# Performance work log

Measured on AMD Instinct MI355X. Metric: run time of the kernel, lower is better.

## Reference

```python
import jax, jax.numpy as jnp
import numpy as np

B, S, HID = 2, 1024, 2048
NH, NKV, D = 16, 8, 128
EPS = 1e-4 / 65535.0  # observer eps from ConcatObserver


def _ste(x, dq):
    # straight-through estimator used by torch fake-quant
    return x + jax.lax.stop_gradient(dq - x)


def _fq_range(x, mn, mx):
    # 16-bit per-tensor affine quantize-dequantize over a given range
    scale = jnp.maximum((mx - mn) / 65535.0, EPS)
    zp = jnp.round(-mn / scale)
    q = jnp.clip(jnp.round(x / scale) + zp, 0.0, 65535.0)
    return _ste(x, (q - zp) * scale)


def fq16(x):
    # ActivationQDQ(bits=16), per-tensor affine, zero included in range
    mn = jnp.minimum(jnp.min(x), 0.0)
    mx = jnp.maximum(jnp.max(x), 0.0)
    return _fq_range(x, mn, mx)


def fq8_sym(x):
    # ActivationQDQ(bits=8, per_tensor_symmetric)
    scale = jnp.maximum(jnp.max(jnp.abs(x)) / 127.0, 1e-12)
    q = jnp.clip(jnp.round(x / scale), -128.0, 127.0)
    return _ste(x, q * scale)


def lpbq_linear(x, W, block=32, qmax=7.0):
    # QLinearLPBQ: int4 weights with per-(out, block-of-32-inputs) scales, no bias
    O, I = W.shape
    Wb = W.reshape(O, I // block, block)
    s = jnp.maximum(jnp.max(jnp.abs(Wb), axis=-1, keepdims=True) / qmax, 1e-12)
    Wq = (jnp.clip(jnp.round(Wb / s), -qmax - 1.0, qmax) * s).reshape(O, I)
    return x @ _ste(W, Wq).T


def rmsnorm_fq(x, w, eps=1e-6):
    # QRMSNorm(head_dim, quant_bits=16)
    var = jnp.mean(x * x, axis=-1, keepdims=True)
    return fq16(x * jax.lax.rsqrt(var + eps) * w)


def rotate_half_fq(x):
    # rotate_half with neg-half QDQ and concat observer (range = union of observed tensors)
    d = x.shape[-1] // 2
    x1, x2 = x[..., :d], x[..., d:]
    neg = fq16(-x2)
    mn = jnp.minimum(jnp.minimum(jnp.min(x), jnp.min(neg)), 0.0)
    mx = jnp.maximum(jnp.maximum(jnp.max(x), jnp.max(neg)), 0.0)
    return _fq_range(jnp.concatenate([neg, x1], axis=-1), mn, mx)


def _attn_forward(hidden_states, cos, sin, attention_mask, Wq, Wk, Wv, Wo, q_norm_w, k_norm_w):
    scaling = D ** -0.5
    hs = fq16(hidden_states)                                            # q_proj_input_qdq
    q = fq16(lpbq_linear(hs, Wq)).reshape(B, S, NH, D)                  # q_norm_input_qdq
    q = jnp.transpose(rmsnorm_fq(q, q_norm_w), (0, 2, 1, 3))            # [B,NH,S,D]
    k = fq16(lpbq_linear(hs, Wk)).reshape(B, S, NKV, D)                 # k_norm_input_qdq
    k = jnp.transpose(rmsnorm_fq(k, k_norm_w), (0, 2, 1, 3))            # [B,NKV,S,D]
    v = jnp.transpose(lpbq_linear(hs, Wv).reshape(B, S, NKV, D), (0, 2, 1, 3))
    q = fq16(q)                                                         # q_norm_output_qdq
    k = fq16(k)                                                         # k_norm_output_qdq
    c = cos[:, None, :, :]
    s_ = sin[:, None, :, :]
    q = fq16(fq16(q * c) + fq16(rotate_half_fq(q) * s_))                # q RoPE with QDQs
    k = fq16(fq16(k * c) + fq16(rotate_half_fq(k) * s_))                # k RoPE with QDQs
    k = fq8_sym(k)                                                      # k_cast_to_int8_qdq
    v = fq8_sym(fq16(v))                                                # v int16 then int8 QDQ
    k = jnp.repeat(k, NH // NKV, axis=1)                                # repeat_kv
    v = jnp.repeat(v, NH // NKV, axis=1)
    sc = fq16(jnp.full((1,), scaling, dtype=hs.dtype))                  # scaling_qdq
    attn = fq16(fq16(jnp.einsum('bhsd,bhtd->bhst', q, k)) * sc)         # qk_matmul + mul_0
    amin = fq16(jnp.min(attn, axis=-1, keepdims=True))                  # reduce_min_output_qdq
    vv = fq16(amin + fq16(jnp.full((1,), -20.0, dtype=hs.dtype)))       # minus_0 (+ neg_20)
    attn = fq16(jnp.where(attention_mask == 0, attn, vv))               # where_attn_qdq
    attn = fq16(jax.nn.softmax(attn.astype(jnp.float32), axis=-1).astype(hs.dtype))
    out = fq16(jnp.einsum('bhst,bhtd->bhsd', attn, v))                  # attn_value_matmul
    out = jnp.transpose(out, (0, 2, 1, 3)).reshape(B, S, NH * D)
    return lpbq_linear(out, Wo), attn


def setup_inputs() -> dict:
    key = jax.random.key(0)
    ks = jax.random.split(key, 6)
    hidden_states = jax.random.normal(ks[0], (B, S, HID), jnp.float32)
    pos = jnp.arange(S, dtype=jnp.float32)
    inv_freq = 1.0 / (1e6 ** (jnp.arange(0, D, 2, dtype=jnp.float32) / D))
    fr = pos[:, None] * inv_freq[None, :]
    emb = jnp.concatenate([fr, fr], axis=-1)                            # [S, D]
    cos = jnp.broadcast_to(jnp.cos(emb)[None], (B, S, D))
    sin = jnp.broadcast_to(jnp.sin(emb)[None], (B, S, D))
    attention_mask = jnp.triu(jnp.ones((S, S), jnp.int32), 1)[None, None]  # 0=keep (causal)
    Wq = jax.random.normal(ks[1], (NH * D, HID), jnp.float32) * 0.02
    Wk = jax.random.normal(ks[2], (NKV * D, HID), jnp.float32) * 0.02
    Wv = jax.random.normal(ks[3], (NKV * D, HID), jnp.float32) * 0.02
    Wo = jax.random.normal(ks[4], (HID, NH * D), jnp.float32) * 0.02
    q_norm_w = jnp.ones((D,), jnp.float32)
    k_norm_w = jnp.ones((D,), jnp.float32)
    return {"hidden_states": hidden_states, "cos": cos, "sin": sin,
            "attention_mask": attention_mask, "Wq": Wq, "Wk": Wk, "Wv": Wv, "Wo": Wo,
            "q_norm_w": q_norm_w, "k_norm_w": k_norm_w}


def reference(hidden_states, cos, sin, attention_mask, Wq, Wk, Wv, Wo, q_norm_w, k_norm_w):
    return _attn_forward(hidden_states, cos, sin, attention_mask, Wq, Wk, Wv, Wo, q_norm_w, k_norm_w)
```

## Files before the change

kernel.cpp:

```cpp
#include <hip/hip_runtime.h>
#include <cfloat>
#include <cmath>


#define FQ_EPS      1.5259021896696422e-09f
#define SCALING_F   0.08838834764831845f
#define S_LEN       1024

typedef _Float16 h8_t __attribute__((ext_vector_type(8)));
typedef _Float16 h4_t __attribute__((ext_vector_type(4)));
typedef float    f4_t __attribute__((ext_vector_type(4)));
typedef unsigned short u16x4 __attribute__((ext_vector_type(4)));

__device__ __forceinline__ unsigned f2o(float f){
  unsigned u = __float_as_uint(f);
  return (u & 0x80000000u) ? ~u : (u | 0x80000000u);
}
__device__ __forceinline__ float o2f(unsigned u){
  return __uint_as_float((u & 0x80000000u) ? (u ^ 0x80000000u) : ~u);
}
__device__ __forceinline__ float dec_slot(const unsigned* st, int s){ return o2f(st[s*16]); }

struct FQP { float scale, zp, inv; };
__device__ __forceinline__ FQP fqp_raw(float mn, float mx){
  FQP p; p.scale = fmaxf((mx - mn)/65535.0f, FQ_EPS); p.zp = rintf(-mn/p.scale);
  p.inv = 1.0f/p.scale; return p;
}
__device__ __forceinline__ FQP fqp(float mn0, float mx0){
  return fqp_raw(fminf(mn0, 0.0f), fmaxf(mx0, 0.0f));
}
__device__ __forceinline__ float fqa(float x, FQP p){
  float q = rintf(x*p.inv) + p.zp;
  q = fminf(fmaxf(q, 0.0f), 65535.0f);
  return (q - p.zp)*p.scale;
}
__device__ __forceinline__ float fq8(float x, float s, float si){
  return fminf(fmaxf(rintf(x*si), -128.0f), 127.0f)*s;
}

__device__ __forceinline__ float bred_min(float v, float* red){
  int tid = threadIdx.x; red[tid] = v; __syncthreads();
  for (int s = 128; s > 0; s >>= 1){ if (tid < s) red[tid] = fminf(red[tid], red[tid+s]); __syncthreads(); }
  float r = red[0]; __syncthreads(); return r;
}
__device__ __forceinline__ float bred_max(float v, float* red){
  int tid = threadIdx.x; red[tid] = v; __syncthreads();
  for (int s = 128; s > 0; s >>= 1){ if (tid < s) red[tid] = fmaxf(red[tid], red[tid+s]); __syncthreads(); }
  float r = red[0]; __syncthreads(); return r;
}


__global__ void k_init(unsigned* stats){
  int i = blockIdx.x*blockDim.x + threadIdx.x;
  if (i < 1024) stats[i] = (((i & 15) == 0) && (((i >> 4) & 1) == 0)) ? 0xFFFFFFFFu : 0u;
}

__global__ __launch_bounds__(256) void k_quantw4(const float* __restrict__ Wq, const float* __restrict__ Wk,
                                                 const float* __restrict__ Wv, const float* __restrict__ Wo,
                                                 _Float16* __restrict__ Qh, _Float16* __restrict__ Kh,
                                                 _Float16* __restrict__ Vh, _Float16* __restrict__ Oh){
  int bx = blockIdx.x;
  const float* W; _Float16* Wh; int base;
  if (bx < 4096){ W = Wq; Wh = Qh; base = 0; }
  else if (bx < 6144){ W = Wk; Wh = Kh; base = 4096; }
  else if (bx < 8192){ W = Wv; Wh = Vh; base = 6144; }
  else { W = Wo; Wh = Oh; base = 8192; }
  int i = (bx - base)*256 + threadIdx.x;
  float4 v = ((const float4*)W)[i];
  float am = fmaxf(fmaxf(fabsf(v.x), fabsf(v.y)), fmaxf(fabsf(v.z), fabsf(v.w)));
  #pragma unroll
  for (int m = 1; m < 8; m <<= 1) am = fmaxf(am, __shfl_xor(am, m, 64));
  float s = fmaxf(am/7.0f, 1e-12f), si = 1.0f/s;
  h4_t o;
  o[0] = (_Float16)(fminf(fmaxf(rintf(v.x*si), -8.0f), 7.0f)*s);
  o[1] = (_Float16)(fminf(fmaxf(rintf(v.y*si), -8.0f), 7.0f)*s);
  o[2] = (_Float16)(fminf(fmaxf(rintf(v.z*si), -8.0f), 7.0f)*s);
  o[3] = (_Float16)(fminf(fmaxf(rintf(v.w*si), -8.0f), 7.0f)*s);
  *(h4_t*)(Wh + ((size_t)i << 2)) = o;
}

__global__ __launch_bounds__(256) void k_minmax(const float* __restrict__ x, int n, unsigned* stats, int slot){
  float mn = FLT_MAX, mx = -FLT_MAX;
  for (int i = blockIdx.x*256 + threadIdx.x; i < n; i += gridDim.x*256){
    float v = x[i]; mn = fminf(mn, v); mx = fmaxf(mx, v);
  }
  __shared__ float red[256];
  float bmn = bred_min(mn, red), bmx = bred_max(mx, red);
  if (threadIdx.x == 0){ atomicMin(&stats[slot*16], f2o(bmn)); atomicMax(&stats[(slot+1)*16], f2o(bmx)); }
}

__global__ __launch_bounds__(256) void k_fq_ew16(const float* __restrict__ x, _Float16* __restrict__ y,
                                                 const unsigned* stats, int slot){
  FQP p = fqp(dec_slot(stats, slot), dec_slot(stats, slot+1));
  int i = blockIdx.x*256 + threadIdx.x;
  float4 v = ((const float4*)x)[i];
  h4_t o;
  o[0] = (_Float16)fqa(v.x, p); o[1] = (_Float16)fqa(v.y, p);
  o[2] = (_Float16)fqa(v.z, p); o[3] = (_Float16)fqa(v.w, p);
  *(h4_t*)(y + ((size_t)i << 2)) = o;
}

__global__ __launch_bounds__(256) void k_fq8_ew16(const float* __restrict__ x, _Float16* __restrict__ y,
                                                  const unsigned* stats, int slot){
  FQP p = fqp(dec_slot(stats, slot), dec_slot(stats, slot+1));
  float lo = fqa(dec_slot(stats, slot), p), hi = fqa(dec_slot(stats, slot+1), p);
  float s8 = fmaxf(fmaxf(fabsf(lo), fabsf(hi))/127.0f, 1e-12f), s8i = 1.0f/s8;
  int i = blockIdx.x*256 + threadIdx.x;
  float4 v = ((const float4*)x)[i];
  h4_t o;
  o[0] = (_Float16)fq8(fqa(v.x, p), s8, s8i); o[1] = (_Float16)fq8(fqa(v.y, p), s8, s8i);
  o[2] = (_Float16)fq8(fqa(v.z, p), s8, s8i); o[3] = (_Float16)fq8(fqa(v.w, p), s8, s8i);
  *(h4_t*)(y + ((size_t)i << 2)) = o;
}

#define GLDS16(g, l) __builtin_amdgcn_global_load_lds( \
    (__attribute__((address_space(1))) unsigned int*)(g), \
    (__attribute__((address_space(3))) unsigned int*)(l), 16, 0, 0)

__device__ __forceinline__ void stage_tile(const _Float16* __restrict__ src, int ld, int k0,
                                           _Float16* __restrict__ dst){
  #pragma unroll
  for (int it = 0; it < 2; it++){
    int c = threadIdx.x + (it << 8);
    int row = c >> 2, off = (c & 3) << 3;
    GLDS16(src + (size_t)row*ld + k0 + off, dst + (c << 3));
  }
}

__device__ __forceinline__ void hgemm_main(const _Float16* __restrict__ A, int lda,
                                           const _Float16* __restrict__ B, int ldb, int K,
                                           f4_t acc[4][4], _Float16* As, _Float16* Bs){
  int lane = threadIdx.x & 63, wave = threadIdx.x >> 6;
  int wm = wave & 1, wn = wave >> 1, quad = lane >> 4, l15 = lane & 15;
  for (int k0 = 0; k0 < K; k0 += 32){
    __syncthreads();
    stage_tile(A, lda, k0, As);
    stage_tile(B, ldb, k0, Bs);
    __syncthreads();
    h8_t af[4], bf[4];
    #pragma unroll
    for (int mt = 0; mt < 4; mt++)
      af[mt] = *(const h8_t*)(As + ((((wm<<6) + (mt<<4) + l15)) << 5) + (quad << 3));
    #pragma unroll
    for (int nt = 0; nt < 4; nt++)
      bf[nt] = *(const h8_t*)(Bs + ((((wn<<6) + (nt<<4) + l15)) << 5) + (quad << 3));
    #pragma unroll
    for (int mt = 0; mt < 4; mt++)
      #pragma unroll
      for (int nt = 0; nt < 4; nt++)
        acc[mt][nt] = __builtin_amdgcn_mfma_f32_16x16x32_f16(af[mt], bf[nt], acc[mt][nt], 0, 0, 0);
  }
}

#define HG_PROLOG  \
  __shared__ __align__(16) _Float16 As[4096], Bs[4096]; \
  __shared__ float red[256]; \
  f4_t acc[4][4]; \
  { f4_t zz = {0.f,0.f,0.f,0.f}; \
    for (int i=0;i<4;i++) for (int j=0;j<4;j++) acc[i][j] = zz; } \
  int lane = threadIdx.x & 63, wave = threadIdx.x >> 6; \
  int wm = wave & 1, wn = wave >> 1, quad = lane >> 4, l15 = lane & 15; (void)red; (void)lane;


__global__ __launch_bounds__(256) void k_hgemm_f(const _Float16* __restrict__ A, const _Float16* __restrict__ B,
                                                 float* __restrict__ C, int N, int K,
                                                 unsigned* stats, int slotC){
  HG_PROLOG
  int bm = blockIdx.y << 7, bn = blockIdx.x << 7;
  hgemm_main(A + (size_t)bm*K, K, B + (size_t)bn*K, K, K, acc, As, Bs);
  float mn = FLT_MAX, mx = -FLT_MAX;
  #pragma unroll
  for (int mt = 0; mt < 4; mt++)
    #pragma unroll
    for (int nt = 0; nt < 4; nt++){
      int Cc = bn + (wn<<6) + (nt<<4) + l15;
      #pragma unroll
      for (int i = 0; i < 4; i++){
        int R = bm + (wm<<6) + (mt<<4) + (quad<<2) + i;
        float v = acc[mt][nt][i];
        C[(size_t)R*N + Cc] = v;
        mn = fminf(mn, v); mx = fmaxf(mx, v);
      }
    }
  if (slotC >= 0){
    float bmn = bred_min(mn, red), bmx = bred_max(mx, red);
    if (threadIdx.x == 0){ atomicMin(&stats[slotC*16], f2o(bmn)); atomicMax(&stats[(slotC+1)*16], f2o(bmx)); }
  }
}

__global__ __launch_bounds__(256) void k_hgemm_qkv(const _Float16* __restrict__ A,
                                                   const _Float16* __restrict__ Bq,
                                                   const _Float16* __restrict__ Bk,
                                                   const _Float16* __restrict__ Bv,
                                                   float* __restrict__ Cq, float* __restrict__ Ck,
                                                   float* __restrict__ Cv,
                                                   int K, unsigned* stats){
  HG_PROLOG
  int z = blockIdx.z;
  const _Float16* Bmat; float* C; int slotC, N, cbase;
  if (z < 2){ Bmat = Bq + (((size_t)z << 10))*K; C = Cq; slotC = 2; N = 2048; cbase = z << 10; }
  else if (z == 2){ Bmat = Bk; C = Ck; slotC = 4; N = 1024; cbase = 0; }
  else { Bmat = Bv; C = Cv; slotC = 6; N = 1024; cbase = 0; }
  int bm = blockIdx.y << 7, bn = blockIdx.x << 7;
  hgemm_main(A + (size_t)bm*K, K, Bmat + (size_t)bn*K, K, K, acc, As, Bs);
  float mn = FLT_MAX, mx = -FLT_MAX;
  #pragma unroll
  for (int mt = 0; mt < 4; mt++)
    #pragma unroll
    for (int nt = 0; nt < 4; nt++){
      int Cc = cbase + bn + (wn<<6) + (nt<<4) + l15;
      #pragma unroll
      for (int i = 0; i < 4; i++){
        int R = bm + (wm<<6) + (mt<<4) + (quad<<2) + i;
        float v = acc[mt][nt][i];
        C[(size_t)R*N + Cc] = v;
        mn = fminf(mn, v); mx = fmaxf(mx, v);
      }
    }
  float bmn = bred_min(mn, red), bmx = bred_max(mx, red);
  if (threadIdx.x == 0){ atomicMin(&stats[slotC*16], f2o(bmn)); atomicMax(&stats[(slotC+1)*16], f2o(bmx)); }
}


#define QK_IDS \
  int lane = threadIdx.x & 63, wn = threadIdx.x >> 6; \
  int quad = lane >> 4, l15 = lane & 15; \
  int tid = threadIdx.x; (void)tid; (void)lane;

__device__ __forceinline__ void qk_load_a(const _Float16* __restrict__ Ab, int quad, int l15,
                                          h8_t Aq[2][4]){
  #pragma unroll
  for (int mt = 0; mt < 2; mt++)
    #pragma unroll
    for (int k0 = 0; k0 < 4; k0++)
      Aq[mt][k0] = *(const h8_t*)(Ab + (size_t)((mt<<4) + l15)*128 + (k0<<5) + (quad<<3));
}

__device__ __forceinline__ void qk_chunk32(const h8_t Aq[2][4], const _Float16* __restrict__ Kb,
                                           int bn, int wn, int quad, int l15, f4_t acc[2][2]){
  #pragma unroll
  for (int k0 = 0; k0 < 4; k0++){
    h8_t bf[2];
    #pragma unroll
    for (int nt = 0; nt < 2; nt++)
      bf[nt] = *(const h8_t*)(Kb + (size_t)(bn + (wn<<5) + (nt<<4) + l15)*128 + (k0<<5) + (quad<<3));
    #pragma unroll
    for (int mt = 0; mt < 2; mt++)
      #pragma unroll
      for (int nt = 0; nt < 2; nt++)
        acc[mt][nt] = __builtin_amdgcn_mfma_f32_16x16x32_f16(Aq[mt][k0], bf[nt], acc[mt][nt], 0, 0, 0);
  }
}

__global__ __launch_bounds__(256) void k_qk_stats(const _Float16* __restrict__ q_h, const _Float16* __restrict__ k_h,
                                                  unsigned* stats, unsigned* rowmin, unsigned* rowmax){
  QK_IDS
  int bm = blockIdx.x << 5, z = blockIdx.y;
  int b = z >> 4, h = z & 15;
  const _Float16* Ab = q_h + (size_t)z*131072 + (size_t)bm*128;
  const _Float16* Kb = k_h + (size_t)(b*8 + (h>>1))*131072;
  h8_t Aq[2][4];
  qk_load_a(Ab, quad, l15, Aq);
  float rmv[2][4], rxv[2][4];
  #pragma unroll
  for (int mt = 0; mt < 2; mt++)
    #pragma unroll
    for (int i = 0; i < 4; i++){ rmv[mt][i] = FLT_MAX; rxv[mt][i] = -FLT_MAX; }
  float mn = FLT_MAX, mx = -FLT_MAX, mxU = -FLT_MAX;
  for (int bn = 0; bn < 1024; bn += 128){
    f4_t acc[2][2];
    { f4_t zz = {0.f,0.f,0.f,0.f}; for (int i=0;i<2;i++) for (int j=0;j<2;j++) acc[i][j]=zz; }
    qk_chunk32(Aq, Kb, bn, wn, quad, l15, acc);
    #pragma unroll
    for (int mt = 0; mt < 2; mt++){
      int rb = bm + (mt<<4) + (quad<<2);
      #pragma unroll
      for (int nt = 0; nt < 2; nt++){
        int t = bn + (wn<<5) + (nt<<4) + l15;
        #pragma unroll
        for (int i = 0; i < 4; i++){
          float v = acc[mt][nt][i];
          mn = fminf(mn, v); mx = fmaxf(mx, v);
          rmv[mt][i] = fminf(rmv[mt][i], v);
          if (t <= rb + i){ mxU = fmaxf(mxU, v); rxv[mt][i] = fmaxf(rxv[mt][i], v); }
        }
      }
    }
  }
  #pragma unroll
  for (int d = 1; d < 16; d <<= 1)
    #pragma unroll
    for (int mt = 0; mt < 2; mt++)
      #pragma unroll
      for (int i = 0; i < 4; i++){
        rmv[mt][i] = fminf(rmv[mt][i], __shfl_xor(rmv[mt][i], d, 64));
        rxv[mt][i] = fmaxf(rxv[mt][i], __shfl_xor(rxv[mt][i], d, 64));
      }
  __shared__ float rminS[4][32], rmaxS[4][32];
  if (l15 == 0){
    #pragma unroll
    for (int mt = 0; mt < 2; mt++)
      #pragma unroll
      for (int i = 0; i < 4; i++){
        int rl = (mt<<4) + (quad<<2) + i;
        rminS[wn][rl] = rmv[mt][i];
        rmaxS[wn][rl] = rxv[mt][i];
      }
  }
  __syncthreads();
  if (tid < 32){
    float a = fminf(fminf(rminS[0][tid], rminS[1][tid]), fminf(rminS[2][tid], rminS[3][tid]));
    float c = fmaxf(fmaxf(rmaxS[0][tid], rmaxS[1][tid]), fmaxf(rmaxS[2][tid], rmaxS[3][tid]));
    rowmin[(z << 10) + bm + tid] = f2o(a);
    rowmax[(z << 10) + bm + tid] = f2o(c);
  }
  __shared__ float red[256];
  float bmn = bred_min(mn, red), bmx = bred_max(mx, red), bmU = bred_max(mxU, red);
  if (tid == 0){
    atomicMin(&stats[28*16], f2o(bmn));
    atomicMax(&stats[29*16], f2o(bmx));
    atomicMax(&stats[31*16], f2o(bmU));
  }
}

__global__ __launch_bounds__(256) void k_rowstat_m2(const unsigned* __restrict__ rowmin, unsigned* stats, int n){
  float lm = -FLT_MAX;
  for (int i = blockIdx.x*256 + threadIdx.x; i < n; i += gridDim.x*256) lm = fmaxf(lm, o2f(rowmin[i]));
  __shared__ float red[256];
  float m = bred_max(lm, red);
  if (threadIdx.x == 0) atomicMax(&stats[35*16], f2o(m));
}
__global__ __launch_bounds__(256) void k_denom_min(const float* __restrict__ denomS, unsigned* stats, int n){
  float lm = FLT_MAX;
  for (int i = blockIdx.x*256 + threadIdx.x; i < n; i += gridDim.x*256) lm = fminf(lm, denomS[i]);
  __shared__ float red[256];
  float m = -bred_max(-lm, red);
  if (threadIdx.x == 0) atomicMin(&stats[32*16], f2o(m));
}

struct LogitQ { FQP f1, f2, fam, fvv, f3; float sc, c20; };
__device__ LogitQ derive_logit(const unsigned* st){
  LogitQ L;
  FQP ps = fqp(SCALING_F, SCALING_F); L.sc = fqa(SCALING_F, ps);
  FQP p20 = fqp(-20.0f, -20.0f);      L.c20 = fqa(-20.0f, p20);
  float gmn = dec_slot(st, 28), gmx = dec_slot(st, 29);
  float gU = dec_slot(st, 31), M2 = dec_slot(st, 35);
  L.f1 = fqp(gmn, gmx);
  float l1lo = fqa(gmn, L.f1), l1hi = fqa(gmx, L.f1);
  L.f2 = fqp(l1lo*L.sc, l1hi*L.sc);
  float amlo = fqa(fqa(gmn, L.f1)*L.sc, L.f2);
  float amhi = fqa(fqa(M2, L.f1)*L.sc, L.f2);
  L.fam = fqp(amlo, amhi);
  float vslo = fqa(amlo, L.fam) + L.c20, vshi = fqa(amhi, L.fam) + L.c20;
  L.fvv = fqp(vslo, vshi);
  float mn3 = fqa(vslo, L.fvv);
  float mx3 = fqa(fqa(gU, L.f1)*L.sc, L.f2);
  L.f3 = fqp(mn3, mx3);
  return L;
}
__device__ __forceinline__ float chainU(float raw, const LogitQ& L){
  return fqa(fqa(fqa(raw, L.f1)*L.sc, L.f2), L.f3);
}

__global__ __launch_bounds__(256) void k_qk_denom(const _Float16* __restrict__ q_h, const _Float16* __restrict__ k_h,
                                                  const unsigned* __restrict__ rowmin,
                                                  const unsigned* __restrict__ rowmax,
                                                  float* __restrict__ denomS,
                                                  unsigned short* __restrict__ q3buf,
                                                  const unsigned* stats){
  QK_IDS
  int j = blockIdx.x, z = blockIdx.y;
  int b = z >> 4, h = z & 15;
  LogitQ L = derive_logit(stats);
  const _Float16* Kb = k_h + (size_t)(b*8 + (h>>1))*131072;
  __shared__ float mRow[32], vvRow[32], vvLev[32];
  __shared__ float dS[4][32];
  for (int g = 0; g < 2; g++){
    int r = g ? (31 - j) : j;
    int bm = r << 5;
    int nch = (r >> 2) + 1;
    int cstar = (r >> 2) << 7;
    int aa = r >> 2, bb2 = r & 3;
    int cum = (aa + 1)*(2*aa + bb2);
    unsigned short* Qu = q3buf + ((size_t)z*144 + cum)*4096;
    __syncthreads();
    if (tid < 32){
      int row = (z << 10) + bm + tid;
      mRow[tid] = chainU(o2f(rowmax[row]), L);
      float tr = fqa(fqa(o2f(rowmin[row]), L.f1)*L.sc, L.f2);
      float w = fqa(fqa(tr, L.fam) + L.c20, L.fvv);
      float lv = fminf(fmaxf(rintf(w*L.f3.inv) + L.f3.zp, 0.0f), 65535.0f);
      vvLev[tid] = lv;
      vvRow[tid] = (lv - L.f3.zp)*L.f3.scale;
    }
    const _Float16* Ab = q_h + (size_t)z*131072 + (size_t)bm*128;
    h8_t Aq[2][4];
    qk_load_a(Ab, quad, l15, Aq);
    __syncthreads();
    float rs[2][4];
    #pragma unroll
    for (int mt = 0; mt < 2; mt++)
      #pragma unroll
      for (int i = 0; i < 4; i++) rs[mt][i] = 0.0f;
    for (int bn = 0; bn < (nch << 7); bn += 128){
      f4_t acc[2][2];
      { f4_t zz = {0.f,0.f,0.f,0.f}; for (int i=0;i<2;i++) for (int jj=0;jj<2;jj++) acc[i][jj]=zz; }
      qk_chunk32(Aq, Kb, bn, wn, quad, l15, acc);
      unsigned short* Qc = Qu + (size_t)(bn >> 7)*4096;
      if (bn < cstar){
        #pragma unroll
        for (int mt = 0; mt < 2; mt++){
          #pragma unroll
          for (int nt = 0; nt < 2; nt++){
            int cl = (wn<<5) + (nt<<4) + l15;
            #pragma unroll
            for (int i = 0; i < 4; i++){
              int rl = (mt<<4) + (quad<<2) + i;
              float a2 = fqa(fqa(acc[mt][nt][i], L.f1)*L.sc, L.f2);
              float lvl = fminf(fmaxf(rintf(a2*L.f3.inv) + L.f3.zp, 0.0f), 65535.0f);
              Qc[rl*128 + cl] = (unsigned short)lvl;
              float a3 = (lvl - L.f3.zp)*L.f3.scale;
              rs[mt][i] += __expf(a3 - mRow[rl]);
            }
          }
        }
      } else {
        #pragma unroll
        for (int mt = 0; mt < 2; mt++){
          #pragma unroll
          for (int nt = 0; nt < 2; nt++){
            int cl = (wn<<5) + (nt<<4) + l15;
            int t = bn + cl;
            #pragma unroll
            for (int i = 0; i < 4; i++){
              int rl = (mt<<4) + (quad<<2) + i;
              float a2 = fqa(fqa(acc[mt][nt][i], L.f1)*L.sc, L.f2);
              float lvl = fminf(fmaxf(rintf(a2*L.f3.inv) + L.f3.zp, 0.0f), 65535.0f);
              float qs = (t <= bm + rl) ? lvl : vvLev[rl];
              Qc[rl*128 + cl] = (unsigned short)qs;
              float a3 = (qs - L.f3.zp)*L.f3.scale;
              rs[mt][i] += __expf(a3 - mRow[rl]);
            }
          }
        }
      }
    }
    #pragma unroll
    for (int d = 1; d < 16; d <<= 1)
      #pragma unroll
      for (int mt = 0; mt < 2; mt++)
        #pragma unroll
        for (int i = 0; i < 4; i++) rs[mt][i] += __shfl_xor(rs[mt][i], d, 64);
    if (l15 == 0){
      #pragma unroll
      for (int mt = 0; mt < 2; mt++)
        #pragma unroll
        for (int i = 0; i < 4; i++) dS[wn][(mt<<4) + (quad<<2) + i] = rs[mt][i];
    }
    __syncthreads();
    if (tid < 32){
      float nMask = (float)(1024 - (nch << 7));
      denomS[(z << 10) + bm + tid] = (dS[0][tid] + dS[1][tid]) + (dS[2][tid] + dS[3][tid])
                                     + nMask*__expf(vvRow[tid] - mRow[tid]);
    }
  }
}

__global__ __launch_bounds__(256) void k_qk_pv(const unsigned short* __restrict__ q3buf,
                                               const _Float16* __restrict__ vT,
                                               float* __restrict__ ctx,
                                               const unsigned* __restrict__ rowmax,
                                               const float* __restrict__ denomS, unsigned* stats){
  QK_IDS
  int j = blockIdx.x, z = blockIdx.y;
  int b = z >> 4, h = z & 15;
  LogitQ L = derive_logit(stats);
  FQP p4 = fqp(0.0f, 1.0f/dec_slot(stats, 32));
  float c1024 = p4.scale*1024.0f;
  float zp3 = L.f3.zp, s3 = L.f3.scale;
  const _Float16* Vb = vT + (size_t)(b*8 + (h>>1))*131072;
  float* Cb = ctx + ((size_t)b << 10)*2048 + (size_t)h*128;
  float cmn = FLT_MAX, cmx = -FLT_MAX;
  for (int g = 0; g < 2; g++){
    int r = g ? (31 - j) : j;
    int bm = r << 5;
    int nch = (r >> 2) + 1;
    int aa = r >> 2, bb2 = r & 3;
    int cum = (aa + 1)*(2*aa + bb2);
    const unsigned short* Qu = q3buf + ((size_t)z*144 + cum)*4096;
    float mR[2], rpR[2];
    #pragma unroll
    for (int mt = 0; mt < 2; mt++){
      int row = (z << 10) + bm + (mt<<4) + l15;
      mR[mt] = chainU(o2f(rowmax[row]), L);
      rpR[mt] = p4.inv/denomS[row];
    }
    f4_t pacc[2][2];
    { f4_t zz = {0.f,0.f,0.f,0.f}; for (int i=0;i<2;i++) for (int jj=0;jj<2;jj++) pacc[i][jj]=zz; }
    for (int c = 0; c < nch; c++){
      const unsigned short* Qc = Qu + (size_t)c*4096;
      #pragma unroll
      for (int k0 = 0; k0 < 4; k0++){
        h8_t af[2], bf[2];
        #pragma unroll
        for (int mt = 0; mt < 2; mt++){
          const unsigned short* pr = Qc + ((mt<<4) + l15)*128 + (k0<<5) + (quad<<3);
          u16x4 u = *(const u16x4*)pr, w = *(const u16x4*)(pr + 4);
          h8_t o;
          #pragma unroll
          for (int jj = 0; jj < 4; jj++){
            float a3u = ((float)u[jj] - zp3)*s3;
            float nu = fminf(fmaxf(rintf(__expf(a3u - mR[mt])*rpR[mt]), 0.0f), 65535.0f);
            o[jj] = (_Float16)(nu*c1024);
            float a3w = ((float)w[jj] - zp3)*s3;
            float nw = fminf(fmaxf(rintf(__expf(a3w - mR[mt])*rpR[mt]), 0.0f), 65535.0f);
            o[jj+4] = (_Float16)(nw*c1024);
          }
          af[mt] = o;
        }
        #pragma unroll
        for (int nt = 0; nt < 2; nt++)
          bf[nt] = *(const h8_t*)(Vb + (size_t)((wn<<5) + (nt<<4) + l15)*1024 + (c<<7) + (k0<<5) + (quad<<3));
        #pragma unroll
        for (int mt = 0; mt < 2; mt++)
          #pragma unroll
          for (int nt = 0; nt < 2; nt++)
            pacc[mt][nt] = __builtin_amdgcn_mfma_f32_16x16x32_f16(af[mt], bf[nt], pacc[mt][nt], 0, 0, 0);
      }
    }
    #pragma unroll
    for (int mt = 0; mt < 2; mt++)
      #pragma unroll
      for (int nt = 0; nt < 2; nt++){
        int Cc = (wn<<5) + (nt<<4) + l15;
        #pragma unroll
        for (int i = 0; i < 4; i++){
          int R = bm + (mt<<4) + (quad<<2) + i;
          float v = pacc[mt][nt][i]*(1.0f/1024.0f);
          Cb[(size_t)R*2048 + Cc] = v;
          cmn = fminf(cmn, v); cmx = fmaxf(cmx, v);
        }
      }
  }
  __shared__ float red[256];
  float bmn = bred_min(cmn, red), bmx = bred_max(cmx, red);
  if (tid == 0){ atomicMin(&stats[36*16], f2o(bmn)); atomicMax(&stats[37*16], f2o(bmx)); }
}

__global__ __launch_bounds__(256) void k_attn_expand(const unsigned short* __restrict__ q3buf,
                                                     float* __restrict__ attn,
                                                     const unsigned* __restrict__ rowmax,
                                                     const float* __restrict__ denomS,
                                                     const unsigned* stats){
  int c = blockIdx.x, r = blockIdx.y, z = blockIdx.z;
  int nch = (r >> 2) + 1;
  int tid = threadIdx.x;
  float* Cb = attn + ((size_t)z << 20) + ((size_t)(r << 5))*1024 + (c << 7);
  if (c >= nch){
    f4_t zz = {0.f,0.f,0.f,0.f};
    #pragma unroll
    for (int it = 0; it < 4; it++){
      int idx = (it << 8) + tid;
      int row = idx >> 5, col = (idx & 31) << 2;
      __builtin_nontemporal_store(zz, (f4_t*)(Cb + (size_t)row*1024 + col));
    }
    return;
  }
  LogitQ L = derive_logit(stats);
  FQP p4 = fqp(0.0f, 1.0f/dec_slot(stats, 32));
  float zp3 = L.f3.zp, s3 = L.f3.scale;
  int aa = r >> 2, bb2 = r & 3;
  int cum = (aa + 1)*(2*aa + bb2);
  const unsigned short* Qu = q3buf + ((size_t)z*144 + cum + c)*4096;
  #pragma unroll
  for (int it = 0; it < 4; it++){
    int idx = (it << 8) + tid;
    int row = idx >> 5, col = (idx & 31) << 2;
    int grow = (z << 10) + (r << 5) + row;
    float m = chainU(o2f(rowmax[grow]), L);
    float rp = p4.inv/denomS[grow];
    u16x4 u = *(const u16x4*)(Qu + row*128 + col);
    f4_t v4;
    #pragma unroll
    for (int jj = 0; jj < 4; jj++){
      float a3 = ((float)u[jj] - zp3)*s3;
      float n = fminf(fmaxf(rintf(__expf(a3 - m)*rp), 0.0f), 65535.0f);
      v4[jj] = n*p4.scale;
    }
    __builtin_nontemporal_store(v4, (f4_t*)(Cb + (size_t)row*1024 + col));
  }
}


__global__ __launch_bounds__(256) void k_rms(const float* __restrict__ lin, float* __restrict__ buf,
                                             const float* __restrict__ gw, unsigned* stats,
                                             int slot_lin, int slot_out, int NHh, int rows){
  FQP pA = fqp(dec_slot(stats, slot_lin), dec_slot(stats, slot_lin+1));
  int lane = threadIdx.x & 63;
  int wv = (blockIdx.x*256 + threadIdx.x) >> 6;
  int nwv = (gridDim.x*256) >> 6;
  float w0 = gw[lane], w1 = gw[lane + 64];
  float fmn = FLT_MAX, fmx = -FLT_MAX, hmn = FLT_MAX, hmx = -FLT_MAX;
  for (int r = wv; r < rows; r += nwv){
    int h = r % NHh; int rem = r / NHh; int s2 = rem & 1023; int b = rem >> 10;
    const float* src = lin + (size_t)r*128;
    float x0 = fqa(src[lane], pA), x1 = fqa(src[lane + 64], pA);
    float ss = x0*x0 + x1*x1;
    #pragma unroll
    for (int m = 1; m < 64; m <<= 1) ss += __shfl_xor(ss, m, 64);
    float rr = 1.0f/sqrtf(ss*(1.0f/128.0f) + 1e-6f);
    float y0 = x0*rr*w0, y1 = x1*rr*w1;
    float* dst = buf + ((size_t)((b*NHh + h) << 10) + s2)*128;
    dst[lane] = y0; dst[lane + 64] = y1;
    fmn = fminf(fmn, fminf(y0, y1)); fmx = fmaxf(fmx, fmaxf(y0, y1));
    hmn = fminf(hmn, y1); hmx = fmaxf(hmx, y1);
  }
  __shared__ float red[256];
  float a = bred_min(fmn, red), bb = bred_max(fmx, red);
  float c = bred_min(hmn, red), d = bred_max(hmx, red);
  if (threadIdx.x == 0){
    atomicMin(&stats[slot_out*16], f2o(a));     atomicMax(&stats[(slot_out+1)*16], f2o(bb));
    atomicMin(&stats[(slot_out+2)*16], f2o(c)); atomicMax(&stats[(slot_out+3)*16], f2o(d));
  }
}

struct RopeQ { FQP B, C, E, F; };
__device__ RopeQ derive_rope(const unsigned* st, int base){
  float ymn = dec_slot(st, base),   ymx = dec_slot(st, base+1);
  float y2mn = dec_slot(st, base+2), y2mx = dec_slot(st, base+3);
  RopeQ r;
  r.B = fqp(ymn, ymx);
  float zmn = fqa(ymn, r.B), zmx = fqa(ymx, r.B);
  r.C = fqp(zmn, zmx);
  float zlo = fqa(zmn, r.C), zhi = fqa(zmx, r.C);
  float z2lo = fqa(fqa(y2mn, r.B), r.C), z2hi = fqa(fqa(y2mx, r.B), r.C);
  r.E = fqp(-z2hi, -z2lo);
  float nlo = fqa(-z2hi, r.E), nhi = fqa(-z2lo, r.E);
  r.F = fqp_raw(fminf(fminf(zlo, nlo), 0.0f), fmaxf(fmaxf(zhi, nhi), 0.0f));
  return r;
}

__global__ __launch_bounds__(256) void k_rope(float* __restrict__ buf, const float* __restrict__ cosp,
                                              const float* __restrict__ sinp, unsigned* stats,
                                              int slot_norm, int slot_prod, int slot_sum,
                                              int NHh, int rows, int do_write){
  RopeQ R = derive_rope(stats, slot_norm);
  FQP pD, pG;
  if (do_write){
    pD = fqp(dec_slot(stats, slot_prod),   dec_slot(stats, slot_prod+1));
    pG = fqp(dec_slot(stats, slot_prod+2), dec_slot(stats, slot_prod+3));
  }
  int lane = threadIdx.x & 63;
  int wv = (blockIdx.x*256 + threadIdx.x) >> 6, nwv = (gridDim.x*256) >> 6;
  float m0 = FLT_MAX, M0 = -FLT_MAX, m1 = FLT_MAX, M1 = -FLT_MAX;
  for (int r = wv; r < rows; r += nwv){
    int s2 = r & 1023; int bh = r >> 10; int b = bh/NHh;
    float* base = buf + (size_t)r*128;
    float y0 = base[lane], y1 = base[lane + 64];
    float z0 = fqa(fqa(y0, R.B), R.C), z1 = fqa(fqa(y1, R.B), R.C);
    const float* cr = cosp + (size_t)((b << 10) + s2)*128;
    const float* sr = sinp + (size_t)((b << 10) + s2)*128;
    float c0 = cr[lane], c1 = cr[lane + 64], sn0 = sr[lane], sn1 = sr[lane + 64];
    float pc0 = z0*c0, pc1 = z1*c1;
    float rh0 = fqa(fqa(-z1, R.E), R.F);
    float rh1 = fqa(z0, R.F);
    float ps0 = rh0*sn0, ps1 = rh1*sn1;
    if (!do_write){
      m0 = fminf(m0, fminf(pc0, pc1)); M0 = fmaxf(M0, fmaxf(pc0, pc1));
      m1 = fminf(m1, fminf(ps0, ps1)); M1 = fmaxf(M1, fmaxf(ps0, ps1));
    } else {
      float sv0 = fqa(pc0, pD) + fqa(ps0, pG);
      float sv1 = fqa(pc1, pD) + fqa(ps1, pG);
      base[lane] = sv0; base[lane + 64] = sv1;
      m0 = fminf(m0, fminf(sv0, sv1)); M0 = fmaxf(M0, fmaxf(sv0, sv1));
    }
  }
  __shared__ float red[256];
  if (!do_write){
    float a = bred_min(m0, red), bb = bred_max(M0, red);
    float c = bred_min(m1, red), d = bred_max(M1, red);
    if (threadIdx.x == 0){
      atomicMin(&stats[slot_prod*16], f2o(a));     atomicMax(&stats[(slot_prod+1)*16], f2o(bb));
      atomicMin(&stats[(slot_prod+2)*16], f2o(c)); atomicMax(&stats[(slot_prod+3)*16], f2o(d));
    }
  } else {
    float a = bred_min(m0, red), bb = bred_max(M0, red);
    if (threadIdx.x == 0){ atomicMin(&stats[slot_sum*16], f2o(a)); atomicMax(&stats[(slot_sum+1)*16], f2o(bb)); }
  }
}

__global__ __launch_bounds__(256) void k_vT(const float* __restrict__ vlin, _Float16* __restrict__ vT,
                                            const unsigned* stats){
  FQP pv = fqp(dec_slot(stats, 6), dec_slot(stats, 7));
  float vlo = fqa(dec_slot(stats, 6), pv), vhi = fqa(dec_slot(stats, 7), pv);
  float v8s = fmaxf(fmaxf(fabsf(vlo), fabsf(vhi))/127.0f, 1e-12f), v8si = 1.0f/v8s;
  __shared__ float tile[64][65];
  int bkv = blockIdx.z, t0 = blockIdx.x << 6, d0 = blockIdx.y << 6;
  int b = bkv >> 3, kv = bkv & 7;
  const float* src = vlin + ((size_t)(b << 10))*1024 + (size_t)kv*128;
  int tx = threadIdx.x & 63, tq = threadIdx.x >> 6;
  #pragma unroll
  for (int i = 0; i < 16; i++){
    int tt = (i << 2) + tq;
    float x = src[(size_t)(t0 + tt)*1024 + d0 + tx];
    tile[tx][tt] = fq8(fqa(x, pv), v8s, v8si);
  }
  __syncthreads();
  _Float16* dst = vT + (size_t)bkv*131072;
  #pragma unroll
  for (int i = 0; i < 16; i++){
    int dd = (i << 2) + tq;
    dst[(size_t)(d0 + dd)*1024 + t0 + tx] = (_Float16)tile[dd][tx];
  }
}

extern "C" void kernel_launch(void* const* d_in, const int* in_sizes, int n_in,
                              void* d_out, int out_size, void* d_ws, size_t ws_size,
                              hipStream_t stream){
  (void)in_sizes; (void)n_in; (void)out_size; (void)ws_size;
  const float* hs   = (const float*)d_in[0];
  const float* cosp = (const float*)d_in[1];
  const float* sinp = (const float*)d_in[2];
  const float* Wq   = (const float*)d_in[4];
  const float* Wk   = (const float*)d_in[5];
  const float* Wv   = (const float*)d_in[6];
  const float* Wo   = (const float*)d_in[7];
  const float* qnw  = (const float*)d_in[8];
  const float* knw  = (const float*)d_in[9];

  float* outp = (float*)d_out;
  float* attn = outp + 4194304;

  const size_t MEG = 1u << 20;
  float* wsf = (float*)d_ws;
  _Float16* woq_h = (_Float16*)(wsf + 0);
  _Float16* wqq_h = (_Float16*)(wsf + 2*MEG);
  _Float16* wkq_h = (_Float16*)(wsf + 4*MEG);
  _Float16* wvq_h = (_Float16*)(wsf + 5*MEG);
  _Float16* hsq_h = (_Float16*)(wsf + 6*MEG);
  float* qlin = wsf + 8*MEG;  float* ctx = qlin;
  float* klin = wsf + 12*MEG;
  float* vlin = wsf + 14*MEG;
  float* qbuf = wsf + 16*MEG;
  float* kbuf = wsf + 20*MEG;
  _Float16* q_h   = (_Float16*)(wsf + 22*MEG);
  _Float16* k_h   = (_Float16*)(wsf + 24*MEG);
  _Float16* vT_h  = (_Float16*)(wsf + 25*MEG);
  _Float16* ctx_h = (_Float16*)(wsf + 26*MEG);
  unsigned* rowmin = (unsigned*)(wsf + 28*MEG);
  unsigned* rowmax = (unsigned*)(wsf + 28*MEG + 32768);
  float* denomS = wsf + 28*MEG + 65536;
  unsigned* stats = (unsigned*)(wsf + 28*MEG + 98304);
  unsigned short* q3buf = (unsigned short*)(wsf + 12*MEG);

  k_init<<<4, 256, 0, stream>>>(stats);

  k_quantw4<<<12288, 256, 0, stream>>>(Wq, Wk, Wv, Wo, wqq_h, wkq_h, wvq_h, woq_h);

  k_minmax<<<1024, 256, 0, stream>>>(hs, 4194304, stats, 0);
  k_fq_ew16<<<4096, 256, 0, stream>>>(hs, hsq_h, stats, 0);

  k_hgemm_qkv<<<dim3(8, 16, 4), 256, 0, stream>>>(hsq_h, wqq_h, wkq_h, wvq_h,
                                                  qlin, klin, vlin, 2048, stats);

  k_rms<<<1024, 256, 0, stream>>>(qlin, qbuf, qnw, stats, 2, 8, 16, 32768);
  k_rms<<<512, 256, 0, stream>>>(klin, kbuf, knw, stats, 4, 12, 8, 16384);

  k_rope<<<1024, 256, 0, stream>>>(qbuf, cosp, sinp, stats, 8, 16, 24, 16, 32768, 0);
  k_rope<<<512, 256, 0, stream>>>(kbuf, cosp, sinp, stats, 12, 20, 26, 8, 16384, 0);
  k_rope<<<1024, 256, 0, stream>>>(qbuf, cosp, sinp, stats, 8, 16, 24, 16, 32768, 1);
  k_rope<<<512, 256, 0, stream>>>(kbuf, cosp, sinp, stats, 12, 20, 26, 8, 16384, 1);

  k_fq_ew16<<<4096, 256, 0, stream>>>(qbuf, q_h, stats, 24);
  k_fq8_ew16<<<2048, 256, 0, stream>>>(kbuf, k_h, stats, 26);
  k_vT<<<dim3(16, 2, 16), 256, 0, stream>>>(vlin, vT_h, stats);

  k_qk_stats<<<dim3(32, 32), 256, 0, stream>>>(q_h, k_h, stats, rowmin, rowmax);
  k_rowstat_m2<<<8, 256, 0, stream>>>(rowmin, stats, 32768);
  k_qk_denom<<<dim3(16, 32), 256, 0, stream>>>(q_h, k_h, rowmin, rowmax, denomS, q3buf, stats);
  k_denom_min<<<8, 256, 0, stream>>>(denomS, stats, 32768);
  k_qk_pv<<<dim3(16, 32), 256, 0, stream>>>(q3buf, vT_h, ctx, rowmax, denomS, stats);
  k_attn_expand<<<dim3(8, 32, 32), 256, 0, stream>>>(q3buf, attn, rowmax, denomS, stats);

  k_fq_ew16<<<4096, 256, 0, stream>>>(ctx, ctx_h, stats, 36);
  k_hgemm_f<<<dim3(16, 16), 256, 0, stream>>>(ctx_h, woq_h, outp, 2048, 2048, stats, -1);
}
```

Baseline: 642.8 us.

## Merge Q/K rope and quant launches, retile output GEMM, hoist QK stat reductions

Q and K rope passes and the Q/K fake-quant conversions are each merged into single launches that branch on block index, cutting launch count and letting the small K grids overlap with Q work. The output projection GEMM gets its own kernel with 128x64 tiles, doubling the block count from 256 to 512 for better CU occupancy, and drops the unused stats epilogue. In k_qk_stats the per-element global min/max tracking is replaced by a running per-row max, with the tensor-wide reductions done once after the row reductions. This trades a few extra registers and shuffles for fewer ops in the inner loop.

```diff
diff --git a/kernel.cpp b/kernel.cpp
--- a/kernel.cpp
+++ b/kernel.cpp
@@ -100,17 +100,29 @@
   *(h4_t*)(y + ((size_t)i << 2)) = o;
 }
 
-__global__ __launch_bounds__(256) void k_fq8_ew16(const float* __restrict__ x, _Float16* __restrict__ y,
-                                                  const unsigned* stats, int slot){
-  FQP p = fqp(dec_slot(stats, slot), dec_slot(stats, slot+1));
-  float lo = fqa(dec_slot(stats, slot), p), hi = fqa(dec_slot(stats, slot+1), p);
-  float s8 = fmaxf(fmaxf(fabsf(lo), fabsf(hi))/127.0f, 1e-12f), s8i = 1.0f/s8;
-  int i = blockIdx.x*256 + threadIdx.x;
-  float4 v = ((const float4*)x)[i];
-  h4_t o;
-  o[0] = (_Float16)fq8(fqa(v.x, p), s8, s8i); o[1] = (_Float16)fq8(fqa(v.y, p), s8, s8i);
-  o[2] = (_Float16)fq8(fqa(v.z, p), s8, s8i); o[3] = (_Float16)fq8(fqa(v.w, p), s8, s8i);
-  *(h4_t*)(y + ((size_t)i << 2)) = o;
+__global__ __launch_bounds__(256) void k_fq_qk(const float* __restrict__ qbuf, const float* __restrict__ kbuf,
+                                               _Float16* __restrict__ q_h, _Float16* __restrict__ k_h,
+                                               const unsigned* stats){
+  int bx = blockIdx.x;
+  if (bx < 4096){
+    FQP p = fqp(dec_slot(stats, 24), dec_slot(stats, 25));
+    int i = bx*256 + threadIdx.x;
+    float4 v = ((const float4*)qbuf)[i];
+    h4_t o;
+    o[0] = (_Float16)fqa(v.x, p); o[1] = (_Float16)fqa(v.y, p);
+    o[2] = (_Float16)fqa(v.z, p); o[3] = (_Float16)fqa(v.w, p);
+    *(h4_t*)(q_h + ((size_t)i << 2)) = o;
+  } else {
+    FQP p = fqp(dec_slot(stats, 26), dec_slot(stats, 27));
+    float lo = fqa(dec_slot(stats, 26), p), hi = fqa(dec_slot(stats, 27), p);
+    float s8 = fmaxf(fmaxf(fabsf(lo), fabsf(hi))/127.0f, 1e-12f), s8i = 1.0f/s8;
+    int i = (bx - 4096)*256 + threadIdx.x;
+    float4 v = ((const float4*)kbuf)[i];
+    h4_t o;
+    o[0] = (_Float16)fq8(fqa(v.x, p), s8, s8i); o[1] = (_Float16)fq8(fqa(v.y, p), s8, s8i);
+    o[2] = (_Float16)fq8(fqa(v.z, p), s8, s8i); o[3] = (_Float16)fq8(fqa(v.w, p), s8, s8i);
+    *(h4_t*)(k_h + ((size_t)i << 2)) = o;
+  }
 }
 
 #define GLDS16(g, l) __builtin_amdgcn_global_load_lds( \
@@ -161,32 +173,6 @@
   int lane = threadIdx.x & 63, wave = threadIdx.x >> 6; \
   int wm = wave & 1, wn = wave >> 1, quad = lane >> 4, l15 = lane & 15; (void)red; (void)lane;
 
-
-__global__ __launch_bounds__(256) void k_hgemm_f(const _Float16* __restrict__ A, const _Float16* __restrict__ B,
-                                                 float* __restrict__ C, int N, int K,
-                                                 unsigned* stats, int slotC){
-  HG_PROLOG
-  int bm = blockIdx.y << 7, bn = blockIdx.x << 7;
-  hgemm_main(A + (size_t)bm*K, K, B + (size_t)bn*K, K, K, acc, As, Bs);
-  float mn = FLT_MAX, mx = -FLT_MAX;
-  #pragma unroll
-  for (int mt = 0; mt < 4; mt++)
-    #pragma unroll
-    for (int nt = 0; nt < 4; nt++){
-      int Cc = bn + (wn<<6) + (nt<<4) + l15;
-      #pragma unroll
-      for (int i = 0; i < 4; i++){
-        int R = bm + (wm<<6) + (mt<<4) + (quad<<2) + i;
-        float v = acc[mt][nt][i];
-        C[(size_t)R*N + Cc] = v;
-        mn = fminf(mn, v); mx = fmaxf(mx, v);
-      }
-    }
-  if (slotC >= 0){
-    float bmn = bred_min(mn, red), bmx = bred_max(mx, red);
-    if (threadIdx.x == 0){ atomicMin(&stats[slotC*16], f2o(bmn)); atomicMax(&stats[(slotC+1)*16], f2o(bmx)); }
-  }
-}
 
 __global__ __launch_bounds__(256) void k_hgemm_qkv(const _Float16* __restrict__ A,
                                                    const _Float16* __restrict__ Bq,
@@ -221,6 +207,51 @@
   if (threadIdx.x == 0){ atomicMin(&stats[slotC*16], f2o(bmn)); atomicMax(&stats[(slotC+1)*16], f2o(bmx)); }
 }
 
+__global__ __launch_bounds__(256) void k_hgemm_o(const _Float16* __restrict__ A,
+                                                 const _Float16* __restrict__ B,
+                                                 float* __restrict__ C){
+  __shared__ __align__(16) _Float16 As[4096], Bs[2048];
+  f4_t acc[4][2];
+  { f4_t zz = {0.f,0.f,0.f,0.f};
+    for (int i = 0; i < 4; i++) for (int j = 0; j < 2; j++) acc[i][j] = zz; }
+  int lane = threadIdx.x & 63, wave = threadIdx.x >> 6;
+  int wm = wave & 1, wn = wave >> 1, quad = lane >> 4, l15 = lane & 15;
+  int bm = blockIdx.y << 7, bn = blockIdx.x << 6;
+  const _Float16* Ab = A + (size_t)bm*2048;
+  const _Float16* Bb = B + (size_t)bn*2048;
+  for (int k0 = 0; k0 < 2048; k0 += 32){
+    __syncthreads();
+    stage_tile(Ab, 2048, k0, As);
+    { int c = threadIdx.x;
+      int row = c >> 2, off = (c & 3) << 3;
+      GLDS16(Bb + (size_t)row*2048 + k0 + off, Bs + (c << 3)); }
+    __syncthreads();
+    h8_t af[4], bf[2];
+    #pragma unroll
+    for (int mt = 0; mt < 4; mt++)
+      af[mt] = *(const h8_t*)(As + ((((wm<<6) + (mt<<4) + l15)) << 5) + (quad << 3));
+    #pragma unroll
+    for (int nt = 0; nt < 2; nt++)
+      bf[nt] = *(const h8_t*)(Bs + ((((wn<<5) + (nt<<4) + l15)) << 5) + (quad << 3));
+    #pragma unroll
+    for (int mt = 0; mt < 4; mt++)
+      #pragma unroll
+      for (int nt = 0; nt < 2; nt++)
+        acc[mt][nt] = __builtin_amdgcn_mfma_f32_16x16x32_f16(af[mt], bf[nt], acc[mt][nt], 0, 0, 0);
+  }
+  #pragma unroll
+  for (int mt = 0; mt < 4; mt++)
+    #pragma unroll
+    for (int nt = 0; nt < 2; nt++){
+      int Cc = bn + (wn<<5) + (nt<<4) + l15;
+      #pragma unroll
+      for (int i = 0; i < 4; i++){
+        int R = bm + (wm<<6) + (mt<<4) + (quad<<2) + i;
+        C[(size_t)R*2048 + Cc] = acc[mt][nt][i];
+      }
+    }
+}
+
 
 #define QK_IDS \
   int lane = threadIdx.x & 63, wn = threadIdx.x >> 6; \
@@ -261,12 +292,11 @@
   const _Float16* Kb = k_h + (size_t)(b*8 + (h>>1))*131072;
   h8_t Aq[2][4];
   qk_load_a(Ab, quad, l15, Aq);
-  float rmv[2][4], rxv[2][4];
+  float rmv[2][4], rxa[2][4], rxv[2][4];
   #pragma unroll
   for (int mt = 0; mt < 2; mt++)
     #pragma unroll
-    for (int i = 0; i < 4; i++){ rmv[mt][i] = FLT_MAX; rxv[mt][i] = -FLT_MAX; }
-  float mn = FLT_MAX, mx = -FLT_MAX, mxU = -FLT_MAX;
+    for (int i = 0; i < 4; i++){ rmv[mt][i] = FLT_MAX; rxa[mt][i] = -FLT_MAX; rxv[mt][i] = -FLT_MAX; }
   for (int bn = 0; bn < 1024; bn += 128){
     f4_t acc[2][2];
     { f4_t zz = {0.f,0.f,0.f,0.f}; for (int i=0;i<2;i++) for (int j=0;j<2;j++) acc[i][j]=zz; }
@@ -280,9 +310,9 @@
         #pragma unroll
         for (int i = 0; i < 4; i++){
           float v = acc[mt][nt][i];
-          mn = fminf(mn, v); mx = fmaxf(mx, v);
           rmv[mt][i] = fminf(rmv[mt][i], v);
-          if (t <= rb + i){ mxU = fmaxf(mxU, v); rxv[mt][i] = fmaxf(rxv[mt][i], v); }
+          rxa[mt][i] = fmaxf(rxa[mt][i], v);
+          if (t <= rb + i) rxv[mt][i] = fmaxf(rxv[mt][i], v);
         }
       }
     }
@@ -294,6 +324,7 @@
       #pragma unroll
       for (int i = 0; i < 4; i++){
         rmv[mt][i] = fminf(rmv[mt][i], __shfl_xor(rmv[mt][i], d, 64));
+        rxa[mt][i] = fmaxf(rxa[mt][i], __shfl_xor(rxa[mt][i], d, 64));
         rxv[mt][i] = fmaxf(rxv[mt][i], __shfl_xor(rxv[mt][i], d, 64));
       }
   __shared__ float rminS[4][32], rmaxS[4][32];
@@ -314,6 +345,15 @@
     rowmin[(z << 10) + bm + tid] = f2o(a);
     rowmax[(z << 10) + bm + tid] = f2o(c);
   }
+  float mn = FLT_MAX, mx = -FLT_MAX, mxU = -FLT_MAX;
+  #pragma unroll
+  for (int mt = 0; mt < 2; mt++)
+    #pragma unroll
+    for (int i = 0; i < 4; i++){
+      mn = fminf(mn, rmv[mt][i]);
+      mx = fmaxf(mx, rxa[mt][i]);
+      mxU = fmaxf(mxU, rxv[mt][i]);
+    }
   __shared__ float red[256];
   float bmn = bred_min(mn, red), bmx = bred_max(mx, red), bmU = bred_max(mxU, red);
   if (tid == 0){
@@ -640,10 +680,15 @@
   return r;
 }
 
-__global__ __launch_bounds__(256) void k_rope(float* __restrict__ buf, const float* __restrict__ cosp,
-                                              const float* __restrict__ sinp, unsigned* stats,
-                                              int slot_norm, int slot_prod, int slot_sum,
-                                              int NHh, int rows, int do_write){
+__global__ __launch_bounds__(256) void k_rope(float* __restrict__ bufq, float* __restrict__ bufk,
+                                              const float* __restrict__ cosp, const float* __restrict__ sinp,
+                                              unsigned* stats, int do_write){
+  int isK = (blockIdx.x >= 1024);
+  float* buf = isK ? bufk : bufq;
+  int slot_norm = isK ? 12 : 8, slot_prod = isK ? 20 : 16, slot_sum = isK ? 26 : 24;
+  int NHh = isK ? 8 : 16, rows = isK ? 16384 : 32768;
+  int bid = isK ? (blockIdx.x - 1024) : blockIdx.x;
+  int nblk = isK ? 512 : 1024;
   RopeQ R = derive_rope(stats, slot_norm);
   FQP pD, pG;
   if (do_write){
@@ -651,7 +696,7 @@
     pG = fqp(dec_slot(stats, slot_prod+2), dec_slot(stats, slot_prod+3));
   }
   int lane = threadIdx.x & 63;
-  int wv = (blockIdx.x*256 + threadIdx.x) >> 6, nwv = (gridDim.x*256) >> 6;
+  int wv = (bid*256 + threadIdx.x) >> 6, nwv = (nblk*256) >> 6;
   float m0 = FLT_MAX, M0 = -FLT_MAX, m1 = FLT_MAX, M1 = -FLT_MAX;
   for (int r = wv; r < rows; r += nwv){
     int s2 = r & 1023; int bh = r >> 10; int b = bh/NHh;
@@ -766,13 +811,10 @@
   k_rms<<<1024, 256, 0, stream>>>(qlin, qbuf, qnw, stats, 2, 8, 16, 32768);
   k_rms<<<512, 256, 0, stream>>>(klin, kbuf, knw, stats, 4, 12, 8, 16384);
 
-  k_rope<<<1024, 256, 0, stream>>>(qbuf, cosp, sinp, stats, 8, 16, 24, 16, 32768, 0);
-  k_rope<<<512, 256, 0, stream>>>(kbuf, cosp, sinp, stats, 12, 20, 26, 8, 16384, 0);
-  k_rope<<<1024, 256, 0, stream>>>(qbuf, cosp, sinp, stats, 8, 16, 24, 16, 32768, 1);
-  k_rope<<<512, 256, 0, stream>>>(kbuf, cosp, sinp, stats, 12, 20, 26, 8, 16384, 1);
-
-  k_fq_ew16<<<4096, 256, 0, stream>>>(qbuf, q_h, stats, 24);
-  k_fq8_ew16<<<2048, 256, 0, stream>>>(kbuf, k_h, stats, 26);
+  k_rope<<<1536, 256, 0, stream>>>(qbuf, kbuf, cosp, sinp, stats, 0);
+  k_rope<<<1536, 256, 0, stream>>>(qbuf, kbuf, cosp, sinp, stats, 1);
+
+  k_fq_qk<<<6144, 256, 0, stream>>>(qbuf, kbuf, q_h, k_h, stats);
   k_vT<<<dim3(16, 2, 16), 256, 0, stream>>>(vlin, vT_h, stats);
 
   k_qk_stats<<<dim3(32, 32), 256, 0, stream>>>(q_h, k_h, stats, rowmin, rowmax);
@@ -783,5 +825,5 @@
   k_attn_expand<<<dim3(8, 32, 32), 256, 0, stream>>>(q3buf, attn, rowmax, denomS, stats);
 
   k_fq_ew16<<<4096, 256, 0, stream>>>(ctx, ctx_h, stats, 36);
-  k_hgemm_f<<<dim3(16, 16), 256, 0, stream>>>(ctx_h, woq_h, outp, 2048, 2048, stats, -1);
-}
+  k_hgemm_o<<<dim3(32, 16), 256, 0, stream>>>(ctx_h, woq_h, outp);
+}
```

Result: faster. 595.3 us (-7.4%).
